# Performance work log

Hardware: AMD Instinct MI355X
Metric: run time of the kernel (lower is better)

The kernel has to match this reference:

```python
import jax, jax.numpy as jnp
import numpy as np


def setup_inputs() -> dict:
    key = jax.random.key(0)
    k1, k2, k3, k4 = jax.random.split(key, 4)
    T, E, H, I = 256, 16, 2048, 1024
    x = jax.random.normal(k1, (T, H), dtype=jnp.float32)
    router_logits = jax.random.normal(k2, (T, E), dtype=jnp.float32)
    # dequantized GGUF expert weights (math after dequant is plain fp GEMM)
    w1 = jax.random.normal(k3, (E, 2 * I, H), dtype=jnp.float32) * 0.02  # gate/up fused
    w2 = jax.random.normal(k4, (E, H, I), dtype=jnp.float32) * 0.02     # down proj
    return {"x": x, "router_logits": router_logits, "w1": w1, "w2": w2, "top_k": 4}


def reference(x, router_logits, w1, w2, top_k):
    # Router: softmax -> top-k -> renormalize (vLLM fused_moe default)
    probs = jax.nn.softmax(router_logits, axis=-1)            # [T, E]
    topk_vals, topk_idx = jax.lax.top_k(probs, top_k)          # [T, k]
    topk_vals = topk_vals / jnp.sum(topk_vals, axis=-1, keepdims=True)
    T, E = router_logits.shape
    # dense routing weights (zero for non-selected experts)
    route_w = jnp.zeros((T, E), dtype=x.dtype).at[
        jnp.arange(T)[:, None], topk_idx].set(topk_vals)       # [T, E]

    I = w1.shape[1] // 2
    # gate_up projection for all experts: [T, E, 2I]
    h = jnp.einsum('th,eih->tei', x, w1)
    gate, up = h[..., :I], h[..., I:]
    act = jax.nn.silu(gate) * up                               # silu_and_mul [T, E, I]
    # down projection: [T, E, H]
    y = jnp.einsum('tei,ehi->teh', act, w2)
    # combine with routing weights
    out = jnp.einsum('te,teh->th', route_w, y)                 # [T, H]
    return out
```

## Files before the change

### kernel.cpp

```cpp
#include <hip/hip_runtime.h>


typedef __attribute__((ext_vector_type(8))) short bf16x8;
typedef __attribute__((ext_vector_type(4))) float floatx4;

#define T_TOK 256
#define N_EXP 16
#define H_DIM 2048
#define I_DIM 1024
#define MAX_SLOTS 256

__device__ __forceinline__ short f2bf(float f) {
    union { float f; unsigned u; } v; v.f = f;
    unsigned r = (v.u + 0x7FFFu + ((v.u >> 16) & 1u)) >> 16;
    return (short)r;
}
__device__ __forceinline__ float bf2f(short s) {
    union { unsigned u; float f; } v; v.u = ((unsigned)(unsigned short)s) << 16;
    return v.f;
}
__device__ __forceinline__ bf16x8 pack8(const float* __restrict__ p) {
    float4 a = *(const float4*)p, b = *(const float4*)(p + 4);
    bf16x8 r;
    r[0] = f2bf(a.x); r[1] = f2bf(a.y); r[2] = f2bf(a.z); r[3] = f2bf(a.w);
    r[4] = f2bf(b.x); r[5] = f2bf(b.y); r[6] = f2bf(b.z); r[7] = f2bf(b.w);
    return r;
}

__global__ __launch_bounds__(256) void convert_x_kernel(
    const float* __restrict__ xf, short* __restrict__ xb)
{
    const int i = (blockIdx.x * 256 + threadIdx.x) * 8;
    *(bf16x8*)(xb + i) = pack8(xf + i);
}

__global__ __launch_bounds__(256) void route_kernel(
    const float* __restrict__ logits,
    const int* __restrict__ topk_ptr,
    int* __restrict__ counts, int* __restrict__ tokens,
    int* __restrict__ tok_e, int* __restrict__ tok_slot, float* __restrict__ tok_wt)
{
    __shared__ int lds_counts[N_EXP];
    const int t = threadIdx.x;
    if (t < N_EXP) lds_counts[t] = 0;
    __syncthreads();

    int K = topk_ptr[0];
    if (K > 8) K = 8;
    if (K < 1) K = 1;

    float l[N_EXP];
    #pragma unroll
    for (int j = 0; j < N_EXP; ++j) l[j] = logits[t * N_EXP + j];

    float M = l[0];
    #pragma unroll
    for (int j = 1; j < N_EXP; ++j) M = fmaxf(M, l[j]);

    int idx[8]; float lv[8]; unsigned used = 0u;
    for (int k = 0; k < K; ++k) {
        int bi = 0; float bv = -1e30f;
        #pragma unroll
        for (int j = 0; j < N_EXP; ++j)
            if (!((used >> j) & 1u) && l[j] > bv) { bv = l[j]; bi = j; }
        used |= 1u << bi;
        idx[k] = bi; lv[k] = bv;
    }
    float w[8], s = 0.f;
    for (int k = 0; k < K; ++k) { w[k] = __expf(lv[k] - M); s += w[k]; }
    const float inv = 1.0f / s;

    for (int k = 0; k < K; ++k) {
        const int e = idx[k];
        const int slot = atomicAdd(&lds_counts[e], 1);
        tokens[e * MAX_SLOTS + slot] = t;
        tok_e[t * 8 + k] = e; tok_slot[t * 8 + k] = slot; tok_wt[t * 8 + k] = w[k] * inv;
    }
    __syncthreads();
    if (t < N_EXP) counts[t] = lds_counts[t];
}

__global__ __launch_bounds__(256) void gemm1_kernel(
    const short* __restrict__ xb,
    const float* __restrict__ w1,
    const int* __restrict__ counts, const int* __restrict__ tokens,
    short* __restrict__ act)
{
    const int e = blockIdx.x;
    const int count = counts[e];
    if (count == 0) return;
    const int wave = (int)(threadIdx.x >> 6), lane = (int)(threadIdx.x & 63);
    const int nl = lane & 15, quad = lane >> 4;
    const int i_base = blockIdx.y * 64 + wave * 16;

    const float* wg = w1 + ((size_t)e * H_DIM + (i_base + nl)) * H_DIM;
    const float* wu = w1 + ((size_t)e * H_DIM + (I_DIM + i_base + nl)) * H_DIM;
    const int* toks = tokens + e * MAX_SLOTS;

    for (int ms = 0; ms < count; ms += 128) {
        const short* xr[8];
        #pragma unroll
        for (int mt = 0; mt < 8; ++mt) {
            int s = ms + mt * 16 + nl;
            if (s >= count) s = count - 1;
            xr[mt] = xb + (size_t)toks[s] * H_DIM;
        }
        floatx4 ag[8], au[8];
        #pragma unroll
        for (int mt = 0; mt < 8; ++mt) { ag[mt] = (floatx4)0.0f; au[mt] = (floatx4)0.0f; }

        for (int k = 0; k < H_DIM; k += 32) {
            const int ko = k + quad * 8;
            bf16x8 bg = pack8(wg + ko);
            bf16x8 bu = pack8(wu + ko);
            #pragma unroll
            for (int mt = 0; mt < 8; ++mt) {
                bf16x8 a = *(const bf16x8*)(xr[mt] + ko);
                ag[mt] = __builtin_amdgcn_mfma_f32_16x16x32_bf16(a, bg, ag[mt], 0, 0, 0);
                au[mt] = __builtin_amdgcn_mfma_f32_16x16x32_bf16(a, bu, au[mt], 0, 0, 0);
            }
        }
        #pragma unroll
        for (int mt = 0; mt < 8; ++mt) {
            #pragma unroll
            for (int r = 0; r < 4; ++r) {
                const int slot = ms + mt * 16 + quad * 4 + r;
                if (slot < count) {
                    const float g = ag[mt][r], u = au[mt][r];
                    const float a = g / (1.0f + __expf(-g)) * u;
                    act[(size_t)(e * MAX_SLOTS + slot) * I_DIM + i_base + nl] = f2bf(a);
                }
            }
        }
    }
}

__global__ __launch_bounds__(256) void gemm2_kernel(
    const short* __restrict__ act,
    const float* __restrict__ w2,
    const int* __restrict__ counts,
    short* __restrict__ y)
{
    const int e = blockIdx.x;
    const int count = counts[e];
    if (count == 0) return;
    const int wave = (int)(threadIdx.x >> 6), lane = (int)(threadIdx.x & 63);
    const int nl = lane & 15, quad = lane >> 4;
    const int h_base = blockIdx.y * 64 + wave * 16;

    const float* wr = w2 + ((size_t)e * H_DIM + h_base + nl) * I_DIM;
    const short* acte = act + (size_t)e * MAX_SLOTS * I_DIM;

    for (int ms = 0; ms < count; ms += 128) {
        const short* ar[8];
        #pragma unroll
        for (int mt = 0; mt < 8; ++mt) {
            int s = ms + mt * 16 + nl;
            if (s >= count) s = count - 1;
            ar[mt] = acte + (size_t)s * I_DIM;
        }
        floatx4 acc[8];
        #pragma unroll
        for (int mt = 0; mt < 8; ++mt) acc[mt] = (floatx4)0.0f;

        for (int k = 0; k < I_DIM; k += 32) {
            const int ko = k + quad * 8;
            bf16x8 b = pack8(wr + ko);
            #pragma unroll
            for (int mt = 0; mt < 8; ++mt) {
                bf16x8 a = *(const bf16x8*)(ar[mt] + ko);
                acc[mt] = __builtin_amdgcn_mfma_f32_16x16x32_bf16(a, b, acc[mt], 0, 0, 0);
            }
        }
        #pragma unroll
        for (int mt = 0; mt < 8; ++mt) {
            #pragma unroll
            for (int r = 0; r < 4; ++r) {
                const int slot = ms + mt * 16 + quad * 4 + r;
                if (slot < count)
                    y[(size_t)(e * MAX_SLOTS + slot) * H_DIM + h_base + nl] = f2bf(acc[mt][r]);
            }
        }
    }
}

__global__ __launch_bounds__(256) void gather_kernel(
    const short* __restrict__ y, const int* __restrict__ topk_ptr,
    const int* __restrict__ tok_e, const int* __restrict__ tok_slot,
    const float* __restrict__ tok_wt, float* __restrict__ out)
{
    const int t = blockIdx.x;
    int K = topk_ptr[0];
    if (K > 8) K = 8;
    if (K < 1) K = 1;
    int e[8], sl[8]; float w[8];
    for (int k = 0; k < K; ++k) {
        e[k] = tok_e[t * 8 + k]; sl[k] = tok_slot[t * 8 + k]; w[k] = tok_wt[t * 8 + k];
    }
    for (int h = threadIdx.x; h < H_DIM; h += 256) {
        float s = 0.f;
        for (int k = 0; k < K; ++k)
            s += w[k] * bf2f(y[(size_t)(e[k] * MAX_SLOTS + sl[k]) * H_DIM + h]);
        out[(size_t)t * H_DIM + h] = s;
    }
}

extern "C" void kernel_launch(void* const* d_in, const int* in_sizes, int n_in,
                              void* d_out, int out_size, void* d_ws, size_t ws_size,
                              hipStream_t stream)
{
    const float* x  = (const float*)d_in[0];
    const float* rl = (const float*)d_in[1];
    const float* w1 = (const float*)d_in[2];
    const float* w2 = (const float*)d_in[3];
    const int* topk = (const int*)d_in[4];

    char* ws = (char*)d_ws;
    int*   counts   = (int*)  (ws + 0);
    int*   tokens   = (int*)  (ws + 256);
    int*   tok_e    = (int*)  (ws + 16640);
    int*   tok_slot = (int*)  (ws + 24832);
    float* tok_wt   = (float*)(ws + 33024);
    short* xb       = (short*)(ws + 65536);
    short* act      = (short*)(ws + 1114112);
    short* yb       = (short*)(ws + 9502720);

    convert_x_kernel<<<256, 256, 0, stream>>>(x, xb);
    route_kernel<<<1, 256, 0, stream>>>(rl, topk, counts, tokens, tok_e, tok_slot, tok_wt);
    gemm1_kernel<<<dim3(N_EXP, 16), 256, 0, stream>>>(xb, w1, counts, tokens, act);
    gemm2_kernel<<<dim3(N_EXP, 32), 256, 0, stream>>>(act, w2, counts, yb);
    gather_kernel<<<T_TOK, 256, 0, stream>>>(yb, topk, tok_e, tok_slot, tok_wt, (float*)d_out);
}
```

Baseline: 598.9 us.

## Split K across two wave groups with LDS reduction and templated M-tile count

Both expert GEMM kernels now run 512 threads per block, with two groups of four waves each taking half of the K dimension. Partial accumulators are summed through shared memory before the SiLU/store epilogue. The M-tile loop is templated on the number of active 16-row tiles, so experts with few tokens skip wasted MFMAs and loads. Loads are hoisted ahead of the packing and MFMAs to overlap memory latency. This doubles the waves available to hide the latency of the fp32 weight stream, at the cost of LDS traffic and two barriers per M chunk.

```diff
diff --git a/kernel.cpp b/kernel.cpp
--- a/kernel.cpp
+++ b/kernel.cpp
@@ -19,12 +19,14 @@
     union { unsigned u; float f; } v; v.u = ((unsigned)(unsigned short)s) << 16;
     return v.f;
 }
-__device__ __forceinline__ bf16x8 pack8(const float* __restrict__ p) {
-    float4 a = *(const float4*)p, b = *(const float4*)(p + 4);
+__device__ __forceinline__ bf16x8 pack2f4(float4 a, float4 b) {
     bf16x8 r;
     r[0] = f2bf(a.x); r[1] = f2bf(a.y); r[2] = f2bf(a.z); r[3] = f2bf(a.w);
     r[4] = f2bf(b.x); r[5] = f2bf(b.y); r[6] = f2bf(b.z); r[7] = f2bf(b.w);
     return r;
+}
+__device__ __forceinline__ bf16x8 pack8(const float* __restrict__ p) {
+    return pack2f4(*(const float4*)p, *(const float4*)(p + 4));
 }
 
 __global__ __launch_bounds__(256) void convert_x_kernel(
@@ -80,106 +82,182 @@
     if (t < N_EXP) counts[t] = lds_counts[t];
 }
 
-__global__ __launch_bounds__(256) void gemm1_kernel(
+template<int MT>
+__device__ __forceinline__ void g1_ms(
+    int ms, int count, const int* __restrict__ toks, const short* __restrict__ xb,
+    const float* __restrict__ wg, const float* __restrict__ wu,
+    int quad, int nl, int lane, int iw, int kh, int i_base, int e,
+    short* __restrict__ act, floatx4* red)
+{
+    const short* xr[MT];
+    #pragma unroll
+    for (int mt = 0; mt < MT; ++mt) {
+        int s = ms + mt * 16 + nl;
+        if (s >= count) s = count - 1;
+        xr[mt] = xb + (size_t)toks[s] * H_DIM + kh * (H_DIM / 2);
+    }
+    floatx4 ag[MT], au[MT];
+    #pragma unroll
+    for (int mt = 0; mt < MT; ++mt) { ag[mt] = (floatx4)0.0f; au[mt] = (floatx4)0.0f; }
+
+    for (int k = 0; k < H_DIM / 2; k += 32) {
+        const int ko = k + quad * 8;
+        float4 g0 = *(const float4*)(wg + ko), g1 = *(const float4*)(wg + ko + 4);
+        float4 u0 = *(const float4*)(wu + ko), u1 = *(const float4*)(wu + ko + 4);
+        bf16x8 av[MT];
+        #pragma unroll
+        for (int mt = 0; mt < MT; ++mt) av[mt] = *(const bf16x8*)(xr[mt] + ko);
+        bf16x8 bg = pack2f4(g0, g1);
+        bf16x8 bu = pack2f4(u0, u1);
+        #pragma unroll
+        for (int mt = 0; mt < MT; ++mt) {
+            ag[mt] = __builtin_amdgcn_mfma_f32_16x16x32_bf16(av[mt], bg, ag[mt], 0, 0, 0);
+            au[mt] = __builtin_amdgcn_mfma_f32_16x16x32_bf16(av[mt], bu, au[mt], 0, 0, 0);
+        }
+    }
+    if (kh) {
+        #pragma unroll
+        for (int mt = 0; mt < MT; ++mt) {
+            red[(((iw * 8 + mt) * 2 + 0) * 64) + lane] = ag[mt];
+            red[(((iw * 8 + mt) * 2 + 1) * 64) + lane] = au[mt];
+        }
+    }
+    __syncthreads();
+    if (!kh) {
+        #pragma unroll
+        for (int mt = 0; mt < MT; ++mt) {
+            floatx4 g = ag[mt] + red[(((iw * 8 + mt) * 2 + 0) * 64) + lane];
+            floatx4 u = au[mt] + red[(((iw * 8 + mt) * 2 + 1) * 64) + lane];
+            #pragma unroll
+            for (int r = 0; r < 4; ++r) {
+                const int slot = ms + mt * 16 + quad * 4 + r;
+                if (slot < count) {
+                    const float gv = g[r], uv = u[r];
+                    const float a = gv / (1.0f + __expf(-gv)) * uv;
+                    act[(size_t)(e * MAX_SLOTS + slot) * I_DIM + i_base + nl] = f2bf(a);
+                }
+            }
+        }
+    }
+    __syncthreads();
+}
+
+__global__ __launch_bounds__(512, 2) void gemm1_kernel(
     const short* __restrict__ xb,
     const float* __restrict__ w1,
     const int* __restrict__ counts, const int* __restrict__ tokens,
     short* __restrict__ act)
 {
+    __shared__ floatx4 red[4 * 8 * 2 * 64];
     const int e = blockIdx.x;
     const int count = counts[e];
     if (count == 0) return;
-    const int wave = (int)(threadIdx.x >> 6), lane = (int)(threadIdx.x & 63);
+    const int tid = (int)threadIdx.x;
+    const int wave = tid >> 6, lane = tid & 63;
+    const int iw = wave & 3, kh = wave >> 2;
     const int nl = lane & 15, quad = lane >> 4;
-    const int i_base = blockIdx.y * 64 + wave * 16;
-
-    const float* wg = w1 + ((size_t)e * H_DIM + (i_base + nl)) * H_DIM;
-    const float* wu = w1 + ((size_t)e * H_DIM + (I_DIM + i_base + nl)) * H_DIM;
+    const int i_base = blockIdx.y * 64 + iw * 16;
+
+    const float* wg = w1 + ((size_t)e * H_DIM + (i_base + nl)) * H_DIM + kh * (H_DIM / 2);
+    const float* wu = w1 + ((size_t)e * H_DIM + (I_DIM + i_base + nl)) * H_DIM + kh * (H_DIM / 2);
     const int* toks = tokens + e * MAX_SLOTS;
 
     for (int ms = 0; ms < count; ms += 128) {
-        const short* xr[8];
-        #pragma unroll
-        for (int mt = 0; mt < 8; ++mt) {
-            int s = ms + mt * 16 + nl;
-            if (s >= count) s = count - 1;
-            xr[mt] = xb + (size_t)toks[s] * H_DIM;
-        }
-        floatx4 ag[8], au[8];
-        #pragma unroll
-        for (int mt = 0; mt < 8; ++mt) { ag[mt] = (floatx4)0.0f; au[mt] = (floatx4)0.0f; }
-
-        for (int k = 0; k < H_DIM; k += 32) {
-            const int ko = k + quad * 8;
-            bf16x8 bg = pack8(wg + ko);
-            bf16x8 bu = pack8(wu + ko);
-            #pragma unroll
-            for (int mt = 0; mt < 8; ++mt) {
-                bf16x8 a = *(const bf16x8*)(xr[mt] + ko);
-                ag[mt] = __builtin_amdgcn_mfma_f32_16x16x32_bf16(a, bg, ag[mt], 0, 0, 0);
-                au[mt] = __builtin_amdgcn_mfma_f32_16x16x32_bf16(a, bu, au[mt], 0, 0, 0);
-            }
-        }
-        #pragma unroll
-        for (int mt = 0; mt < 8; ++mt) {
+        const int rem = count - ms;
+        const int nmt = rem >= 128 ? 8 : ((rem + 15) >> 4);
+        switch (nmt) {
+            case 1: g1_ms<1>(ms, count, toks, xb, wg, wu, quad, nl, lane, iw, kh, i_base, e, act, red); break;
+            case 2: g1_ms<2>(ms, count, toks, xb, wg, wu, quad, nl, lane, iw, kh, i_base, e, act, red); break;
+            case 3: g1_ms<3>(ms, count, toks, xb, wg, wu, quad, nl, lane, iw, kh, i_base, e, act, red); break;
+            case 4: g1_ms<4>(ms, count, toks, xb, wg, wu, quad, nl, lane, iw, kh, i_base, e, act, red); break;
+            case 5: g1_ms<5>(ms, count, toks, xb, wg, wu, quad, nl, lane, iw, kh, i_base, e, act, red); break;
+            case 6: g1_ms<6>(ms, count, toks, xb, wg, wu, quad, nl, lane, iw, kh, i_base, e, act, red); break;
+            case 7: g1_ms<7>(ms, count, toks, xb, wg, wu, quad, nl, lane, iw, kh, i_base, e, act, red); break;
+            default: g1_ms<8>(ms, count, toks, xb, wg, wu, quad, nl, lane, iw, kh, i_base, e, act, red); break;
+        }
+    }
+}
+
+template<int MT>
+__device__ __forceinline__ void g2_ms(
+    int ms, int count, const short* __restrict__ acte,
+    const float* __restrict__ wr,
+    int quad, int nl, int lane, int iw, int kh, int h_base, int e,
+    short* __restrict__ y, floatx4* red)
+{
+    const short* ar[MT];
+    #pragma unroll
+    for (int mt = 0; mt < MT; ++mt) {
+        int s = ms + mt * 16 + nl;
+        if (s >= count) s = count - 1;
+        ar[mt] = acte + (size_t)s * I_DIM + kh * (I_DIM / 2);
+    }
+    floatx4 acc[MT];
+    #pragma unroll
+    for (int mt = 0; mt < MT; ++mt) acc[mt] = (floatx4)0.0f;
+
+    for (int k = 0; k < I_DIM / 2; k += 32) {
+        const int ko = k + quad * 8;
+        float4 b0 = *(const float4*)(wr + ko), b1 = *(const float4*)(wr + ko + 4);
+        bf16x8 av[MT];
+        #pragma unroll
+        for (int mt = 0; mt < MT; ++mt) av[mt] = *(const bf16x8*)(ar[mt] + ko);
+        bf16x8 b = pack2f4(b0, b1);
+        #pragma unroll
+        for (int mt = 0; mt < MT; ++mt)
+            acc[mt] = __builtin_amdgcn_mfma_f32_16x16x32_bf16(av[mt], b, acc[mt], 0, 0, 0);
+    }
+    if (kh) {
+        #pragma unroll
+        for (int mt = 0; mt < MT; ++mt) red[(iw * 8 + mt) * 64 + lane] = acc[mt];
+    }
+    __syncthreads();
+    if (!kh) {
+        #pragma unroll
+        for (int mt = 0; mt < MT; ++mt) {
+            floatx4 a = acc[mt] + red[(iw * 8 + mt) * 64 + lane];
             #pragma unroll
             for (int r = 0; r < 4; ++r) {
                 const int slot = ms + mt * 16 + quad * 4 + r;
-                if (slot < count) {
-                    const float g = ag[mt][r], u = au[mt][r];
-                    const float a = g / (1.0f + __expf(-g)) * u;
-                    act[(size_t)(e * MAX_SLOTS + slot) * I_DIM + i_base + nl] = f2bf(a);
-                }
+                if (slot < count)
+                    y[(size_t)(e * MAX_SLOTS + slot) * H_DIM + h_base + nl] = f2bf(a[r]);
             }
         }
     }
-}
-
-__global__ __launch_bounds__(256) void gemm2_kernel(
+    __syncthreads();
+}
+
+__global__ __launch_bounds__(512, 4) void gemm2_kernel(
     const short* __restrict__ act,
     const float* __restrict__ w2,
     const int* __restrict__ counts,
     short* __restrict__ y)
 {
+    __shared__ floatx4 red[4 * 8 * 64];
     const int e = blockIdx.x;
     const int count = counts[e];
     if (count == 0) return;
-    const int wave = (int)(threadIdx.x >> 6), lane = (int)(threadIdx.x & 63);
+    const int tid = (int)threadIdx.x;
+    const int wave = tid >> 6, lane = tid & 63;
+    const int iw = wave & 3, kh = wave >> 2;
     const int nl = lane & 15, quad = lane >> 4;
-    const int h_base = blockIdx.y * 64 + wave * 16;
-
-    const float* wr = w2 + ((size_t)e * H_DIM + h_base + nl) * I_DIM;
+    const int h_base = blockIdx.y * 64 + iw * 16;
+
+    const float* wr = w2 + ((size_t)e * H_DIM + h_base + nl) * I_DIM + kh * (I_DIM / 2);
     const short* acte = act + (size_t)e * MAX_SLOTS * I_DIM;
 
     for (int ms = 0; ms < count; ms += 128) {
-        const short* ar[8];
-        #pragma unroll
-        for (int mt = 0; mt < 8; ++mt) {
-            int s = ms + mt * 16 + nl;
-            if (s >= count) s = count - 1;
-            ar[mt] = acte + (size_t)s * I_DIM;
-        }
-        floatx4 acc[8];
-        #pragma unroll
-        for (int mt = 0; mt < 8; ++mt) acc[mt] = (floatx4)0.0f;
-
-        for (int k = 0; k < I_DIM; k += 32) {
-            const int ko = k + quad * 8;
-            bf16x8 b = pack8(wr + ko);
-            #pragma unroll
-            for (int mt = 0; mt < 8; ++mt) {
-                bf16x8 a = *(const bf16x8*)(ar[mt] + ko);
-                acc[mt] = __builtin_amdgcn_mfma_f32_16x16x32_bf16(a, b, acc[mt], 0, 0, 0);
-            }
-        }
-        #pragma unroll
-        for (int mt = 0; mt < 8; ++mt) {
-            #pragma unroll
-            for (int r = 0; r < 4; ++r) {
-                const int slot = ms + mt * 16 + quad * 4 + r;
-                if (slot < count)
-                    y[(size_t)(e * MAX_SLOTS + slot) * H_DIM + h_base + nl] = f2bf(acc[mt][r]);
-            }
+        const int rem = count - ms;
+        const int nmt = rem >= 128 ? 8 : ((rem + 15) >> 4);
+        switch (nmt) {
+            case 1: g2_ms<1>(ms, count, acte, wr, quad, nl, lane, iw, kh, h_base, e, y, red); break;
+            case 2: g2_ms<2>(ms, count, acte, wr, quad, nl, lane, iw, kh, h_base, e, y, red); break;
+            case 3: g2_ms<3>(ms, count, acte, wr, quad, nl, lane, iw, kh, h_base, e, y, red); break;
+            case 4: g2_ms<4>(ms, count, acte, wr, quad, nl, lane, iw, kh, h_base, e, y, red); break;
+            case 5: g2_ms<5>(ms, count, acte, wr, quad, nl, lane, iw, kh, h_base, e, y, red); break;
+            case 6: g2_ms<6>(ms, count, acte, wr, quad, nl, lane, iw, kh, h_base, e, y, red); break;
+            case 7: g2_ms<7>(ms, count, acte, wr, quad, nl, lane, iw, kh, h_base, e, y, red); break;
+            default: g2_ms<8>(ms, count, acte, wr, quad, nl, lane, iw, kh, h_base, e, y, red); break;
         }
     }
 }
@@ -227,7 +305,7 @@
 
     convert_x_kernel<<<256, 256, 0, stream>>>(x, xb);
     route_kernel<<<1, 256, 0, stream>>>(rl, topk, counts, tokens, tok_e, tok_slot, tok_wt);
-    gemm1_kernel<<<dim3(N_EXP, 16), 256, 0, stream>>>(xb, w1, counts, tokens, act);
-    gemm2_kernel<<<dim3(N_EXP, 32), 256, 0, stream>>>(act, w2, counts, yb);
+    gemm1_kernel<<<dim3(N_EXP, 16), 512, 0, stream>>>(xb, w1, counts, tokens, act);
+    gemm2_kernel<<<dim3(N_EXP, 32), 512, 0, stream>>>(act, w2, counts, yb);
     gather_kernel<<<T_TOK, 256, 0, stream>>>(yb, topk, tok_e, tok_slot, tok_wt, (float*)d_out);
 }
```

Result: faster. 527.4 us (-11.9%).

## Stage MoE GEMM tiles in LDS with double-buffered prefetch and 512-thread blocks

Applied to the files above, without the earlier changes.

Both expert GEMMs now cooperatively load 128x64 activation and weight tiles into LDS, converting the fp32 weights to bf16 once per tile. The next tile is prefetched into registers while MFMAs run on the current one. Previously each wave read activations straight from global memory with strided gathers. gemm1 now uses 8 waves split between the gate and up halves and combines them through an LDS epilogue. This adds a barrier per k-step and occupies about 72KB of LDS per block, which limits occupancy, and the grid for gemm2 is halved.

```diff
diff --git a/kernel.cpp b/kernel.cpp
--- a/kernel.cpp
+++ b/kernel.cpp
@@ -9,6 +9,11 @@
 #define H_DIM 2048
 #define I_DIM 1024
 #define MAX_SLOTS 256
+#define BK 64
+#define LDW 72
+#define TILE (128 * LDW)
+#define NT1 (H_DIM / BK)
+#define NT2 (I_DIM / BK)
 
 __device__ __forceinline__ short f2bf(float f) {
     union { float f; unsigned u; } v; v.f = f;
@@ -19,12 +24,14 @@
     union { unsigned u; float f; } v; v.u = ((unsigned)(unsigned short)s) << 16;
     return v.f;
 }
-__device__ __forceinline__ bf16x8 pack8(const float* __restrict__ p) {
-    float4 a = *(const float4*)p, b = *(const float4*)(p + 4);
+__device__ __forceinline__ bf16x8 pack2f4(float4 a, float4 b) {
     bf16x8 r;
     r[0] = f2bf(a.x); r[1] = f2bf(a.y); r[2] = f2bf(a.z); r[3] = f2bf(a.w);
     r[4] = f2bf(b.x); r[5] = f2bf(b.y); r[6] = f2bf(b.z); r[7] = f2bf(b.w);
     return r;
+}
+__device__ __forceinline__ bf16x8 pack8(const float* __restrict__ p) {
+    return pack2f4(*(const float4*)p, *(const float4*)(p + 4));
 }
 
 __global__ __launch_bounds__(256) void convert_x_kernel(
@@ -80,107 +87,185 @@
     if (t < N_EXP) counts[t] = lds_counts[t];
 }
 
-__global__ __launch_bounds__(256) void gemm1_kernel(
+__global__ __launch_bounds__(512, 2) void gemm1_kernel(
     const short* __restrict__ xb,
     const float* __restrict__ w1,
     const int* __restrict__ counts, const int* __restrict__ tokens,
     short* __restrict__ act)
 {
+    __shared__ short lds[4 * TILE];
     const int e = blockIdx.x;
     const int count = counts[e];
     if (count == 0) return;
-    const int wave = (int)(threadIdx.x >> 6), lane = (int)(threadIdx.x & 63);
+    const int tid = (int)threadIdx.x;
+    const int wave = tid >> 6, lane = tid & 63;
+    const int gu = wave >> 2, iw = wave & 3;
     const int nl = lane & 15, quad = lane >> 4;
-    const int i_base = blockIdx.y * 64 + wave * 16;
-
-    const float* wg = w1 + ((size_t)e * H_DIM + (i_base + nl)) * H_DIM;
-    const float* wu = w1 + ((size_t)e * H_DIM + (I_DIM + i_base + nl)) * H_DIM;
+    const int i_base = blockIdx.y * 64;
     const int* toks = tokens + e * MAX_SLOTS;
 
+    const int sr = tid >> 2;
+    const int sk = (tid & 3) << 4;
+    const int w1row = i_base + (sr & 63) + ((sr >> 6) << 10);
+    const float* wsrc = w1 + ((size_t)e * H_DIM + w1row) * H_DIM + sk;
+    const int st = sr * LDW + sk;
+
     for (int ms = 0; ms < count; ms += 128) {
-        const short* xr[8];
+        int slotS = ms + sr; if (slotS >= count) slotS = count - 1;
+        const short* asrc = xb + (size_t)toks[slotS] * H_DIM + sk;
+
+        floatx4 acc[8];
         #pragma unroll
-        for (int mt = 0; mt < 8; ++mt) {
-            int s = ms + mt * 16 + nl;
-            if (s >= count) s = count - 1;
-            xr[mt] = xb + (size_t)toks[s] * H_DIM;
-        }
-        floatx4 ag[8], au[8];
-        #pragma unroll
-        for (int mt = 0; mt < 8; ++mt) { ag[mt] = (floatx4)0.0f; au[mt] = (floatx4)0.0f; }
-
-        for (int k = 0; k < H_DIM; k += 32) {
-            const int ko = k + quad * 8;
-            bf16x8 bg = pack8(wg + ko);
-            bf16x8 bu = pack8(wu + ko);
+        for (int mt = 0; mt < 8; ++mt) acc[mt] = (floatx4)0.0f;
+
+        {
+            float4 b0 = *(const float4*)(wsrc + 0), b1 = *(const float4*)(wsrc + 4);
+            float4 b2 = *(const float4*)(wsrc + 8), b3 = *(const float4*)(wsrc + 12);
+            bf16x8 a0 = *(const bf16x8*)(asrc + 0), a1 = *(const bf16x8*)(asrc + 8);
+            *(bf16x8*)(lds + 0 * TILE + st) = a0;
+            *(bf16x8*)(lds + 0 * TILE + st + 8) = a1;
+            *(bf16x8*)(lds + 2 * TILE + st) = pack2f4(b0, b1);
+            *(bf16x8*)(lds + 2 * TILE + st + 8) = pack2f4(b2, b3);
+        }
+        __syncthreads();
+
+        for (int kt = 0; kt < NT1; ++kt) {
+            const int cur = kt & 1, nxt = cur ^ 1;
+            const bool pf = (kt + 1 < NT1);
+            float4 b0, b1, b2, b3; bf16x8 a0, a1;
+            if (pf) {
+                const float* ws = wsrc + (kt + 1) * BK;
+                const short* as = asrc + (kt + 1) * BK;
+                b0 = *(const float4*)(ws + 0);  b1 = *(const float4*)(ws + 4);
+                b2 = *(const float4*)(ws + 8);  b3 = *(const float4*)(ws + 12);
+                a0 = *(const bf16x8*)(as + 0);  a1 = *(const bf16x8*)(as + 8);
+            }
+            const short* A = lds + cur * TILE;
+            const short* B = lds + (2 + cur) * TILE;
+            #pragma unroll
+            for (int c = 0; c < 2; ++c) {
+                bf16x8 bf = *(const bf16x8*)(B + (gu * 64 + iw * 16 + nl) * LDW + c * 32 + quad * 8);
+                #pragma unroll
+                for (int mt = 0; mt < 8; ++mt) {
+                    bf16x8 af = *(const bf16x8*)(A + (mt * 16 + nl) * LDW + c * 32 + quad * 8);
+                    acc[mt] = __builtin_amdgcn_mfma_f32_16x16x32_bf16(af, bf, acc[mt], 0, 0, 0);
+                }
+            }
+            if (pf) {
+                *(bf16x8*)(lds + nxt * TILE + st) = a0;
+                *(bf16x8*)(lds + nxt * TILE + st + 8) = a1;
+                *(bf16x8*)(lds + (2 + nxt) * TILE + st) = pack2f4(b0, b1);
+                *(bf16x8*)(lds + (2 + nxt) * TILE + st + 8) = pack2f4(b2, b3);
+            }
+            __syncthreads();
+        }
+
+        floatx4* epi = (floatx4*)lds;
+        if (gu == 1) {
+            #pragma unroll
+            for (int mt = 0; mt < 8; ++mt) epi[(iw * 8 + mt) * 64 + lane] = acc[mt];
+        }
+        __syncthreads();
+        if (gu == 0) {
             #pragma unroll
             for (int mt = 0; mt < 8; ++mt) {
-                bf16x8 a = *(const bf16x8*)(xr[mt] + ko);
-                ag[mt] = __builtin_amdgcn_mfma_f32_16x16x32_bf16(a, bg, ag[mt], 0, 0, 0);
-                au[mt] = __builtin_amdgcn_mfma_f32_16x16x32_bf16(a, bu, au[mt], 0, 0, 0);
-            }
-        }
-        #pragma unroll
-        for (int mt = 0; mt < 8; ++mt) {
-            #pragma unroll
-            for (int r = 0; r < 4; ++r) {
-                const int slot = ms + mt * 16 + quad * 4 + r;
-                if (slot < count) {
-                    const float g = ag[mt][r], u = au[mt][r];
-                    const float a = g / (1.0f + __expf(-g)) * u;
-                    act[(size_t)(e * MAX_SLOTS + slot) * I_DIM + i_base + nl] = f2bf(a);
+                floatx4 u = epi[(iw * 8 + mt) * 64 + lane];
+                #pragma unroll
+                for (int r = 0; r < 4; ++r) {
+                    const int slot = ms + mt * 16 + quad * 4 + r;
+                    if (slot < count) {
+                        const float g = acc[mt][r], uv = u[r];
+                        const float a = g / (1.0f + __expf(-g)) * uv;
+                        act[(size_t)(e * MAX_SLOTS + slot) * I_DIM + i_base + iw * 16 + nl] = f2bf(a);
+                    }
                 }
             }
         }
-    }
-}
-
-__global__ __launch_bounds__(256) void gemm2_kernel(
+        __syncthreads();
+    }
+}
+
+__global__ __launch_bounds__(512, 2) void gemm2_kernel(
     const short* __restrict__ act,
     const float* __restrict__ w2,
     const int* __restrict__ counts,
     short* __restrict__ y)
 {
+    __shared__ short lds[4 * TILE];
     const int e = blockIdx.x;
     const int count = counts[e];
     if (count == 0) return;
-    const int wave = (int)(threadIdx.x >> 6), lane = (int)(threadIdx.x & 63);
+    const int tid = (int)threadIdx.x;
+    const int wave = tid >> 6, lane = tid & 63;
     const int nl = lane & 15, quad = lane >> 4;
-    const int h_base = blockIdx.y * 64 + wave * 16;
-
-    const float* wr = w2 + ((size_t)e * H_DIM + h_base + nl) * I_DIM;
+    const int h_base = blockIdx.y * 128;
+
+    const int sr = tid >> 2;
+    const int sk = (tid & 3) << 4;
+    const float* wsrc = w2 + ((size_t)e * H_DIM + h_base + sr) * I_DIM + sk;
     const short* acte = act + (size_t)e * MAX_SLOTS * I_DIM;
+    const int st = sr * LDW + sk;
 
     for (int ms = 0; ms < count; ms += 128) {
-        const short* ar[8];
-        #pragma unroll
-        for (int mt = 0; mt < 8; ++mt) {
-            int s = ms + mt * 16 + nl;
-            if (s >= count) s = count - 1;
-            ar[mt] = acte + (size_t)s * I_DIM;
-        }
+        int slotS = ms + sr; if (slotS >= count) slotS = count - 1;
+        const short* asrc = acte + (size_t)slotS * I_DIM + sk;
+
         floatx4 acc[8];
         #pragma unroll
         for (int mt = 0; mt < 8; ++mt) acc[mt] = (floatx4)0.0f;
 
-        for (int k = 0; k < I_DIM; k += 32) {
-            const int ko = k + quad * 8;
-            bf16x8 b = pack8(wr + ko);
-            #pragma unroll
-            for (int mt = 0; mt < 8; ++mt) {
-                bf16x8 a = *(const bf16x8*)(ar[mt] + ko);
-                acc[mt] = __builtin_amdgcn_mfma_f32_16x16x32_bf16(a, b, acc[mt], 0, 0, 0);
-            }
-        }
+        {
+            float4 b0 = *(const float4*)(wsrc + 0), b1 = *(const float4*)(wsrc + 4);
+            float4 b2 = *(const float4*)(wsrc + 8), b3 = *(const float4*)(wsrc + 12);
+            bf16x8 a0 = *(const bf16x8*)(asrc + 0), a1 = *(const bf16x8*)(asrc + 8);
+            *(bf16x8*)(lds + 0 * TILE + st) = a0;
+            *(bf16x8*)(lds + 0 * TILE + st + 8) = a1;
+            *(bf16x8*)(lds + 2 * TILE + st) = pack2f4(b0, b1);
+            *(bf16x8*)(lds + 2 * TILE + st + 8) = pack2f4(b2, b3);
+        }
+        __syncthreads();
+
+        for (int kt = 0; kt < NT2; ++kt) {
+            const int cur = kt & 1, nxt = cur ^ 1;
+            const bool pf = (kt + 1 < NT2);
+            float4 b0, b1, b2, b3; bf16x8 a0, a1;
+            if (pf) {
+                const float* ws = wsrc + (kt + 1) * BK;
+                const short* as = asrc + (kt + 1) * BK;
+                b0 = *(const float4*)(ws + 0);  b1 = *(const float4*)(ws + 4);
+                b2 = *(const float4*)(ws + 8);  b3 = *(const float4*)(ws + 12);
+                a0 = *(const bf16x8*)(as + 0);  a1 = *(const bf16x8*)(as + 8);
+            }
+            const short* A = lds + cur * TILE;
+            const short* B = lds + (2 + cur) * TILE;
+            #pragma unroll
+            for (int c = 0; c < 2; ++c) {
+                bf16x8 bf = *(const bf16x8*)(B + (wave * 16 + nl) * LDW + c * 32 + quad * 8);
+                #pragma unroll
+                for (int mt = 0; mt < 8; ++mt) {
+                    bf16x8 af = *(const bf16x8*)(A + (mt * 16 + nl) * LDW + c * 32 + quad * 8);
+                    acc[mt] = __builtin_amdgcn_mfma_f32_16x16x32_bf16(af, bf, acc[mt], 0, 0, 0);
+                }
+            }
+            if (pf) {
+                *(bf16x8*)(lds + nxt * TILE + st) = a0;
+                *(bf16x8*)(lds + nxt * TILE + st + 8) = a1;
+                *(bf16x8*)(lds + (2 + nxt) * TILE + st) = pack2f4(b0, b1);
+                *(bf16x8*)(lds + (2 + nxt) * TILE + st + 8) = pack2f4(b2, b3);
+            }
+            __syncthreads();
+        }
+
         #pragma unroll
         for (int mt = 0; mt < 8; ++mt) {
             #pragma unroll
             for (int r = 0; r < 4; ++r) {
                 const int slot = ms + mt * 16 + quad * 4 + r;
                 if (slot < count)
-                    y[(size_t)(e * MAX_SLOTS + slot) * H_DIM + h_base + nl] = f2bf(acc[mt][r]);
-            }
-        }
+                    y[(size_t)(e * MAX_SLOTS + slot) * H_DIM + h_base + wave * 16 + nl] = f2bf(acc[mt][r]);
+            }
+        }
+        __syncthreads();
     }
 }
 
@@ -227,7 +312,7 @@
 
     convert_x_kernel<<<256, 256, 0, stream>>>(x, xb);
     route_kernel<<<1, 256, 0, stream>>>(rl, topk, counts, tokens, tok_e, tok_slot, tok_wt);
-    gemm1_kernel<<<dim3(N_EXP, 16), 256, 0, stream>>>(xb, w1, counts, tokens, act);
-    gemm2_kernel<<<dim3(N_EXP, 32), 256, 0, stream>>>(act, w2, counts, yb);
+    gemm1_kernel<<<dim3(N_EXP, 16), 512, 0, stream>>>(xb, w1, counts, tokens, act);
+    gemm2_kernel<<<dim3(N_EXP, 16), 512, 0, stream>>>(act, w2, counts, yb);
     gather_kernel<<<T_TOK, 256, 0, stream>>>(yb, topk, tok_e, tok_slot, tok_wt, (float*)d_out);
 }
```

New measurement: 504.1 us. -15.8%, faster.
